# Kernel optimization log

Hardware: AMD Instinct MI355X
Metric: run time of the kernel (lower is better)

## Reference

```python
import jax, jax.numpy as jnp
import numpy as np

BN_EPS = 1e-3  # keras BatchNormalization default epsilon


def _conv(x, w):
    # x: [B,H,W,Cin], w: [kh,kw,Cin,Cout], stride 1, SAME padding
    return jax.lax.conv_general_dilated(
        x, w, window_strides=(1, 1), padding='SAME',
        dimension_numbers=('NHWC', 'HWIO', 'NHWC'))


def _bn(x, g, b, m, v):
    return (x - m) * jax.lax.rsqrt(v + BN_EPS) * g + b


def _pam(x, wq, bq, wk, bk, wv, bv, gamma):
    # Position attention: softmax over HW x HW similarity of 1x1-conv q/k.
    B, H, W, C = x.shape
    q = (_conv(x, wq) + bq).reshape(B, H * W, -1)   # [B,HW,C/8]
    k = (_conv(x, wk) + bk).reshape(B, H * W, -1)   # [B,HW,C/8]
    v = (_conv(x, wv) + bv).reshape(B, H * W, C)    # [B,HW,C]
    energy = jnp.einsum('bic,bjc->bij', q, k)       # [B,HW,HW]
    att = jax.nn.softmax(energy, axis=-1)
    out = jnp.einsum('bij,bjc->bic', att, v).reshape(B, H, W, C)
    return gamma * out + x


def _cam(x, gamma):
    # Channel attention with max-subtract stabilization, softmax over C.
    B, H, W, C = x.shape
    X = x.reshape(B, H * W, C)                      # channel-last flat
    energy = jnp.einsum('bnc,bnd->bcd', X, X)       # [B,C,C]
    energy_new = jnp.max(energy, axis=-1, keepdims=True) - energy
    att = jax.nn.softmax(energy_new, axis=-1)       # [B,C,C]
    out = jnp.einsum('bcd,bnd->bnc', att, X).reshape(B, H, W, C)
    return gamma * out + x


def setup_inputs() -> dict:
    key = jax.random.key(0)
    ks = jax.random.split(key, 16)
    B, H, W = 4, 64, 64
    Cin, Ci, Cq, Cout = 512, 128, 16, 19
    s = 0.05
    d = {
        'x': jax.random.normal(ks[0], (B, H, W, Cin), jnp.float32),
        'w5a': jax.random.normal(ks[1], (3, 3, Cin, Ci), jnp.float32) * s,
        'w5c': jax.random.normal(ks[2], (3, 3, Cin, Ci), jnp.float32) * s,
        'wq': jax.random.normal(ks[3], (1, 1, Ci, Cq), jnp.float32) * s,
        'bq': jnp.zeros((Cq,), jnp.float32),
        'wk': jax.random.normal(ks[4], (1, 1, Ci, Cq), jnp.float32) * s,
        'bk': jnp.zeros((Cq,), jnp.float32),
        'wv': jax.random.normal(ks[5], (1, 1, Ci, Ci), jnp.float32) * s,
        'bv': jnp.zeros((Ci,), jnp.float32),
        'pam_gamma': jnp.float32(0.5),
        'cam_gamma': jnp.float32(0.5),
        'w51': jax.random.normal(ks[6], (3, 3, Ci, Ci), jnp.float32) * s,
        'w52': jax.random.normal(ks[7], (3, 3, Ci, Ci), jnp.float32) * s,
        'w8': jax.random.normal(ks[8], (1, 1, Ci, Cout), jnp.float32) * s,
    }
    for i, nm in enumerate(['bn1', 'bn2', 'bn3', 'bn4']):
        d[nm + '_g'] = jnp.ones((Ci,), jnp.float32)
        d[nm + '_b'] = jnp.zeros((Ci,), jnp.float32)
        d[nm + '_m'] = jax.random.normal(ks[9 + i], (Ci,), jnp.float32) * 0.1
        d[nm + '_v'] = jnp.ones((Ci,), jnp.float32)
    return d


def reference(x, w5a, w5c, wq, bq, wk, bk, wv, bv, pam_gamma, cam_gamma,
              w51, w52, w8,
              bn1_g, bn1_b, bn1_m, bn1_v,
              bn2_g, bn2_b, bn2_m, bn2_v,
              bn3_g, bn3_b, bn3_m, bn3_v,
              bn4_g, bn4_b, bn4_m, bn4_v):
    # PAM branch
    feat1 = jax.nn.relu(_bn(_conv(x, w5a), bn1_g, bn1_b, bn1_m, bn1_v))
    sa_feat = _pam(feat1, wq, bq, wk, bk, wv, bv, pam_gamma)
    sa_conv = jax.nn.relu(_bn(_conv(sa_feat, w51), bn3_g, bn3_b, bn3_m, bn3_v))
    # CAM branch
    feat2 = jax.nn.relu(_bn(_conv(x, w5c), bn2_g, bn2_b, bn2_m, bn2_v))
    sc_feat = _cam(feat2, cam_gamma)
    sc_conv = jax.nn.relu(_bn(_conv(sc_feat, w52), bn4_g, bn4_b, bn4_m, bn4_v))
    # Fused output (dropout is identity at inference)
    feat_sum = sa_conv + sc_conv
    return _conv(feat_sum, w8)
```

## Files before the change

kernel.cpp:

```cpp
#include <hip/hip_runtime.h>
#include <hip/hip_bf16.h>
#include <math.h>

#define BN_EPS 1e-3f
#define LOG2E 1.44269504088896f

constexpr int Bn = 4, Hn = 64, Wn = 64, CIN = 512, CI = 128;
constexpr int HWn = Hn * Wn;
constexpr int NPIX = Bn * HWn;
constexpr int COn = 19;
constexpr int XSL = 66;
constexpr int XPG = XSL * 16;

struct F8 { float4 lo, hi; };

__device__ __forceinline__ F8 f8zero() {
    F8 r; r.lo = make_float4(0.f,0.f,0.f,0.f); r.hi = make_float4(0.f,0.f,0.f,0.f); return r;
}
__device__ __forceinline__ void fma8(F8 &acc, float a, const float4 &wlo, const float4 &whi) {
    acc.lo.x = fmaf(a, wlo.x, acc.lo.x);
    acc.lo.y = fmaf(a, wlo.y, acc.lo.y);
    acc.lo.z = fmaf(a, wlo.z, acc.lo.z);
    acc.lo.w = fmaf(a, wlo.w, acc.lo.w);
    acc.hi.x = fmaf(a, whi.x, acc.hi.x);
    acc.hi.y = fmaf(a, whi.y, acc.hi.y);
    acc.hi.z = fmaf(a, whi.z, acc.hi.z);
    acc.hi.w = fmaf(a, whi.w, acc.hi.w);
}

typedef __attribute__((ext_vector_type(8)))  short    short8;
typedef __attribute__((ext_vector_type(8)))  _Float16 half8;
typedef __attribute__((ext_vector_type(16))) float    f32x16;

__device__ __forceinline__ f32x16 f16z() {
    f32x16 z;
    #pragma unroll
    for (int i = 0; i < 16; ++i) z[i] = 0.f;
    return z;
}
__device__ __forceinline__ unsigned f2b(float f) {
    union { float f; unsigned u; } c; c.f = f;
    return (c.u + 0x7FFFu + ((c.u >> 16) & 1u)) >> 16;
}
__device__ __forceinline__ unsigned pack2(float lo, float hi) {
    return (f2b(hi) << 16) | f2b(lo);
}
__device__ __forceinline__ unsigned pkb2(float a, float b) {
    __hip_bfloat16 ha = __float2bfloat16(a);
    __hip_bfloat16 hb = __float2bfloat16(b);
    return ((unsigned)*(unsigned short*)&hb << 16) | *(unsigned short*)&ha;
}
__device__ __forceinline__ void split2(float a, float b, unsigned &hi, unsigned &lo) {
    const unsigned ha = f2b(a), hb = f2b(b);
    union { unsigned u; float f; } ua, ub; ua.u = ha << 16; ub.u = hb << 16;
    hi = (hb << 16) | ha;
    lo = pack2(a - ua.f, b - ub.f);
}
__device__ __forceinline__ unsigned pkh2(float a, float b) {
    union { _Float16 h; unsigned short u; } ca, cb;
    ca.h = (_Float16)a; cb.h = (_Float16)b;
    return ((unsigned)cb.u << 16) | ca.u;
}

__global__ __launch_bounds__(256)
void k_prep_w(const float* __restrict__ w5a, const float* __restrict__ w5c,
              const float* __restrict__ w51, const float* __restrict__ w52,
              char* __restrict__ wt1F, char* __restrict__ wt2aF, char* __restrict__ wt2bF)
{
    int idx = blockIdx.x * 256 + threadIdx.x;
    if (idx < 589824) {
        const int jp = idx & 7, co = (idx >> 3) & 255, ct = idx >> 11;
        const int tap = ct % 9, c = ct / 9;
        const float* src = (co < 128) ? w5a : w5c;
        const int coc = co & 127;
        const int ci = c*16 + jp*2;
        const float a = src[((size_t)tap*CIN + ci)*CI + coc];
        const float b = src[((size_t)tap*CIN + ci + 1)*CI + coc];
        const int L = co*32 + jp*4;
        *(unsigned*)(wt1F + (size_t)ct*8192 + L) = pkh2(a, b);
    } else {
        int k = idx - 589824;
        if (k >= 147456) return;
        const float* src = (k < 73728) ? w51 : w52;
        char* dstF = (k < 73728) ? wt2aF : wt2bF;
        if (k >= 73728) k -= 73728;
        const int jp = k & 7, co = (k >> 3) & 127, ct = k >> 10;
        const int tap = ct % 9, c = ct / 9;
        const int ci = c*16 + jp*2;
        const float a = src[((size_t)tap*CI + ci)*CI + co];
        const float b = src[((size_t)tap*CI + ci + 1)*CI + co];
        const int L = co*32 + jp*4;
        *(unsigned*)(dstF + (size_t)ct*4096 + L) = pkh2(a, b);
    }
}

__global__ __launch_bounds__(256)
void k_prep_bn(const float* g1, const float* b1, const float* m1, const float* v1,
               const float* g2, const float* b2, const float* m2, const float* v2,
               const float* g3, const float* b3, const float* m3, const float* v3,
               const float* g4, const float* b4, const float* m4, const float* v4,
               float* bnAs, float* bnAb, float* bnBs, float* bnBb)
{
    const int t = threadIdx.x, c = t & 127;
    {
        const float *g = (t < 128) ? g1 : g2, *b = (t < 128) ? b1 : b2;
        const float *m = (t < 128) ? m1 : m2, *v = (t < 128) ? v1 : v2;
        const float s = g[c] * rsqrtf(v[c] + BN_EPS);
        bnAs[t] = s; bnAb[t] = b[c] - m[c]*s;
    }
    {
        const float *g = (t < 128) ? g3 : g4, *b = (t < 128) ? b3 : b4;
        const float *m = (t < 128) ? m3 : m4, *v = (t < 128) ? v3 : v4;
        const float s = g[c] * rsqrtf(v[c] + BN_EPS);
        bnBs[t] = s; bnBb[t] = b[c] - m[c]*s;
    }
}

__global__ __launch_bounds__(256)
void k_prep_x(const float* __restrict__ x, _Float16* __restrict__ xcv)
{
    __shared__ float Xl[16*520];
    const int t = threadIdx.x;
    const int pb = blockIdx.x * 16;
    #pragma unroll
    for (int i = 0; i < 8; ++i) {
        const int u = t + i*256;
        const int px = u >> 7, c4 = (u & 127) * 4;
        *(float4*)&Xl[px*520 + c4] = *(const float4*)&x[(size_t)(pb + px)*CIN + c4];
    }
    __syncthreads();
    const int rowg = pb >> 6, pixb = pb & 63;
    #pragma unroll
    for (int i = 0; i < 8; ++i) {
        const int u = t + i*256;
        const int chunk = u >> 6, rem = u & 63;
        const int pl = rem >> 2, u4 = rem & 3;
        const float* src = &Xl[pl*520 + chunk*16 + u4*4];
        uint2 v;
        v.x = pkh2(src[0], src[1]);
        v.y = pkh2(src[2], src[3]);
        *(uint2*)&xcv[(((size_t)rowg*32 + chunk)*XSL + (pixb + pl + 1))*16 + u4*4] = v;
    }
    if (pixb == 0 && t < 64) {
        const int chunk = t >> 1, sl = (t & 1) * 65;
        uint4* dst = (uint4*)&xcv[(((size_t)rowg*32 + chunk)*XSL + sl)*16];
        uint4 z; z.x = 0u; z.y = 0u; z.z = 0u; z.w = 0u;
        dst[0] = z; dst[1] = z;
    }
}

__global__ __launch_bounds__(256)
void k_zhalo(_Float16* __restrict__ saf_h, _Float16* __restrict__ scf_h)
{
    const int idx = blockIdx.x * 256 + threadIdx.x;
    if (idx >= 8192) return;
    _Float16* arr = (idx & 4096) ? scf_h : saf_h;
    const int rem = idx & 4095;
    const int row = rem >> 4, chunk = (rem >> 1) & 7, sl = (rem & 1) * 65;
    uint4* dst = (uint4*)&arr[(((size_t)row*8 + chunk)*XSL + sl)*16];
    uint4 z; z.x = 0u; z.y = 0u; z.z = 0u; z.w = 0u;
    dst[0] = z; dst[1] = z;
}

template<int NCHNK, int NCOTOT, int WCOBASE>
__global__ __launch_bounds__(256)
void k_convl(const _Float16* __restrict__ xcv0, const _Float16* __restrict__ xcv1,
             const _Float16* __restrict__ wtF0, const _Float16* __restrict__ wtF1,
             const float* __restrict__ bnS, const float* __restrict__ bnBi,
             float* __restrict__ out0, float* __restrict__ out1)
{
    constexpr int WU4  = 1152;
    constexpr int XU4  = 396;
    constexpr int BUFB = (WU4 + XU4) * 16;
    __shared__ __align__(16) char Ls[2*BUFB];

    const int t    = threadIdx.x;
    const int wgid = blockIdx.x;
    const int xcd  = wgid & 7;
    const int sel  = xcd >> 2;
    const int ch2  = (xcd >> 1) & 1;
    const int row  = ((wgid >> 3) << 1) | (xcd & 1);
    const _Float16* xcv = sel ? xcv1 : xcv0;
    const _Float16* wtF = sel ? wtF1 : wtF0;
    float* dst = sel ? out1 : out0;

    const int hh = row & 63;
    const int dyLo = (hh == 0)  ? 1 : 0;
    const int dyHi = (hh == 63) ? 1 : 2;
    const int l = t & 63, w = t >> 6;
    const int lo5 = l & 31, hf = l >> 5;
    const int mi = w >> 1, nt = w & 1;
    const int cobase0 = WCOBASE*sel + ch2*64;

    bool sAct[7]; bool sIsW[7]; int sDst[7]; unsigned sSrc[7]; unsigned sStr[7];
    #pragma unroll
    for (int i = 0; i < 7; ++i) {
        const int u = t + i*256;
        sAct[i] = false; sIsW[i] = false; sDst[i] = -1; sSrc[i] = 0; sStr[i] = 0;
        if (u < WU4) {
            const int tap = u >> 7, rem = u & 127;
            sAct[i] = true; sIsW[i] = true;
            sSrc[i] = (unsigned)((tap*NCOTOT + cobase0)*32 + rem*16);
            sStr[i] = (unsigned)(9*NCOTOT*32);
            sDst[i] = (tap*128 + (rem & 1)*64 + (rem >> 1)) * 16;
        } else if (u < WU4 + XU4) {
            const int j = u - WU4;
            const int page = j / 132, rem132 = j - page*132;
            const int slot = rem132 >> 1, u4h = rem132 & 1;
            sAct[i] = (page >= dyLo && page <= dyHi);
            sSrc[i] = (unsigned)((((row + page - 1)*NCHNK)*XPG + slot*16 + u4h*8) * 2);
            sStr[i] = (unsigned)(XPG*2);
            sDst[i] = (WU4 + j) * 16;
        }
    }
    int xoff[3];
    #pragma unroll
    for (int dx = 0; dx < 3; ++dx)
        xoff[dx] = WU4*16 + ((mi*32 + lo5 + dx)*2 + hf)*16;
    const int wlane = (hf*64 + nt*32 + lo5)*16;

    f32x16 acc = f16z();

    uint4 xr[7];
    auto loadS = [&](int c) {
        #pragma unroll
        for (int i = 0; i < 7; ++i) {
            uint4 v; v.x = 0u; v.y = 0u; v.z = 0u; v.w = 0u;
            if (sAct[i]) {
                const char* base = sIsW[i] ? (const char*)wtF : (const char*)xcv;
                v = *(const uint4*)(base + (size_t)sSrc[i] + (size_t)c*sStr[i]);
            }
            xr[i] = v;
        }
    };

    loadS(0);
    int p = 0;
    for (int c = 0; c < NCHNK; ++c) {
        char* Lp = Ls + p*BUFB;
        #pragma unroll
        for (int i = 0; i < 7; ++i)
            if (sDst[i] >= 0) *(uint4*)(Lp + sDst[i]) = xr[i];
        __syncthreads();
        if (c + 1 < NCHNK) loadS(c + 1);
        #pragma unroll
        for (int dy = 0; dy < 3; ++dy) {
            if (dy < dyLo || dy > dyHi) continue;
            #pragma unroll
            for (int dx = 0; dx < 3; ++dx) {
                const half8 wf = *(const half8*)(Lp + ((dy*3 + dx)*128)*16 + wlane);
                const half8 xf = *(const half8*)(Lp + dy*(132*16) + xoff[dx]);
                acc = __builtin_amdgcn_mfma_f32_32x32x16_f16(wf, xf, acc, 0, 0, 0);
            }
        }
        p ^= 1;
    }
    const int px = mi*32 + lo5;
    const size_t pg = (size_t)row*Wn + px;
    #pragma unroll
    for (int r = 0; r < 16; ++r) {
        const int crow = (r & 3) + 8*(r >> 2) + 4*hf;
        const int och = ch2*64 + nt*32 + crow;
        const int bnidx = sel*128 + och;
        dst[pg*CI + och] = fmaxf(fmaf(acc[r], bnS[bnidx], bnBi[bnidx]), 0.f);
    }
}

__global__ __launch_bounds__(256)
void k_qk(const float* __restrict__ feat1,
          const float* __restrict__ wq, const float* __restrict__ bq,
          const float* __restrict__ wk, const float* __restrict__ bk,
          __hip_bfloat16* __restrict__ qb, __hip_bfloat16* __restrict__ kb)
{
    __shared__ float Al[64*129];
    __shared__ __align__(16) float Wl[128*32];
    const int t = threadIdx.x;
    const int pb = blockIdx.x * 64;
    for (int idx = t; idx < 64*128; idx += 256) {
        const int p = idx >> 7, ci = idx & 127;
        Al[p*129 + ci] = feat1[(size_t)(pb + p)*CI + ci];
    }
    for (int idx = t; idx < 128*32; idx += 256) {
        const int ci = idx >> 5, c = idx & 31;
        Wl[idx] = (c < 16) ? wq[ci*16 + c] : wk[ci*16 + (c - 16)];
    }
    __syncthreads();
    const int p = t & 63, cg = t >> 6, co = cg * 8;
    F8 acc = f8zero();
    #pragma unroll 8
    for (int ci = 0; ci < 128; ++ci) {
        const float a = Al[p*129 + ci];
        const float4 wlo = *(const float4*)&Wl[ci*32 + co];
        const float4 whi = *(const float4*)&Wl[ci*32 + co + 4];
        fma8(acc, a, wlo, whi);
    }
    const float* af = (const float*)&acc;
    #pragma unroll
    for (int j = 0; j < 8; ++j) {
        const int c = co + j;
        if (c < 16) qb[(size_t)(pb + p)*16 + c]        = __float2bfloat16((af[j] + bq[c]) * LOG2E);
        else        kb[(size_t)(pb + p)*16 + (c - 16)] = __float2bfloat16(af[j] + bk[c - 16]);
    }
}

__global__ __launch_bounds__(256)
void k_v(const float* __restrict__ feat1, const float* __restrict__ wv,
         const float* __restrict__ bv, __hip_bfloat16* __restrict__ vbT)
{
    __shared__ float Al[32*129];
    __shared__ __align__(16) float Wl[64*128];
    const int t = threadIdx.x;
    const int pb = blockIdx.x * 32;
    for (int idx = t; idx < 32*128; idx += 256) {
        const int p = idx >> 7, ci = idx & 127;
        Al[p*129 + ci] = feat1[(size_t)(pb + p)*CI + ci];
    }
    const int px = t & 15, co = (t >> 4) * 8;
    F8 acc0 = f8zero(), acc1 = f8zero();
    for (int ch = 0; ch < 2; ++ch) {
        __syncthreads();
        #pragma unroll
        for (int r = 0; r < 8; ++r) {
            const int i4 = t + r*256;
            const int kk = i4 >> 5, c4 = (i4 & 31) * 4;
            *(float4*)&Wl[kk*128 + c4] = *(const float4*)&wv[(size_t)(ch*64 + kk)*CI + c4];
        }
        __syncthreads();
        #pragma unroll 4
        for (int kk = 0; kk < 64; ++kk) {
            const float a0 = Al[px*129 + ch*64 + kk];
            const float a1 = Al[(px+16)*129 + ch*64 + kk];
            const float4 wlo = *(const float4*)&Wl[kk*128 + co];
            const float4 whi = *(const float4*)&Wl[kk*128 + co + 4];
            fma8(acc0, a0, wlo, whi);
            fma8(acc1, a1, wlo, whi);
        }
    }
    const int p0 = pb + px;
    const int bb = p0 / HWn, pin0 = p0 % HWn;
    const int k16a = pin0 >> 4, ko = pin0 & 15;
    const float* a0f = (const float*)&acc0;
    const float* a1f = (const float*)&acc1;
    #pragma unroll
    for (int j = 0; j < 8; ++j) {
        const int c = co + j;
        const size_t base = ((size_t)bb*256*CI*16) + (size_t)c*16 + ko;
        vbT[base + (size_t)k16a*CI*16]       = __float2bfloat16(a0f[j] + bv[c]);
        vbT[base + (size_t)(k16a + 1)*CI*16] = __float2bfloat16(a1f[j] + bv[c]);
    }
}

__global__ __launch_bounds__(256)
void k_pam(const __hip_bfloat16* __restrict__ qb, const __hip_bfloat16* __restrict__ kb,
           const __hip_bfloat16* __restrict__ vbT, const float* __restrict__ feat1,
           const float* __restrict__ gamma, _Float16* __restrict__ saf_h)
{
    __shared__ __align__(16) char pbuf[16896];
    __shared__ float msArr[4][32];
    __shared__ float ssArr[4][32];
    __shared__ float ssum[32];
    const int t  = threadIdx.x;
    const int wv = t >> 6, l = t & 63;
    const int lo5 = l & 31, h = l >> 5;
    unsigned* Ppk = (unsigned*)(pbuf + wv*4096);
    float* osum = (float*)pbuf;

    const int q0 = blockIdx.x * 32;
    const int bb = q0 / HWn;
    const size_t jb = (size_t)bb * HWn;
    const __hip_bfloat16* vbB = vbT + (size_t)bb * 256 * CI * 16;

    const short8 qfrag = *(const short8*)&qb[(size_t)(q0 + lo5)*16 + 8*h];
    const f32x16 zro = f16z();

    f32x16 o[4];
    #pragma unroll
    for (int cb = 0; cb < 4; ++cb) o[cb] = f16z();

    float m_run = -1e30f, s_run = 0.f;

    for (int k0 = wv*1024; k0 < wv*1024 + 1024; k0 += 64) {
        const short8 kf0 = *(const short8*)&kb[(jb + k0 +      lo5)*16 + 8*h];
        const short8 kf1 = *(const short8*)&kb[(jb + k0 + 32 + lo5)*16 + 8*h];
        short8 vf[4][4];
        #pragma unroll
        for (int s = 0; s < 4; ++s)
            #pragma unroll
            for (int cb = 0; cb < 4; ++cb)
                vf[s][cb] = *(const short8*)&vbB[
                    (((size_t)(k0 >> 4) + s)*CI + cb*32 + lo5)*16 + 8*h];

        f32x16 e0 = __builtin_amdgcn_mfma_f32_32x32x16_bf16(kf0, qfrag, zro, 0, 0, 0);
        f32x16 e1 = __builtin_amdgcn_mfma_f32_32x32x16_bf16(kf1, qfrag, zro, 0, 0, 0);

        float mt = fmaxf(e0[0], e1[0]);
        #pragma unroll
        for (int r = 1; r < 16; ++r) mt = fmaxf(mt, fmaxf(e0[r], e1[r]));
        mt = fmaxf(mt, __shfl_xor(mt, 32));

        if (__any(mt > m_run + 11.5416f)) {
            const float mnew = fmaxf(m_run, mt);
            const float sc = exp2f(m_run - mnew);
            s_run *= sc;
            #pragma unroll
            for (int cb = 0; cb < 4; ++cb)
                #pragma unroll
                for (int r = 0; r < 16; ++r) o[cb][r] *= sc;
            m_run = mnew;
        }

        #pragma unroll
        for (int r = 0; r < 16; ++r) {
            e0[r] = exp2f(e0[r] - m_run);
            e1[r] = exp2f(e1[r] - m_run);
        }
        float ss = 0.f;
        #pragma unroll
        for (int r = 0; r < 16; ++r) ss += e0[r] + e1[r];
        s_run += ss;

        #pragma unroll
        for (int r = 0; r < 16; r += 2) {
            const int pidx = ((r & 3) >> 1) + 4*(r >> 2) + 2*h;
            Ppk[pidx*32 + lo5]        = pkb2(e0[r], e0[r+1]);
            Ppk[(16 + pidx)*32 + lo5] = pkb2(e1[r], e1[r+1]);
        }
        #pragma unroll
        for (int s = 0; s < 4; ++s) {
            union { unsigned u[4]; short8 s8; } P;
            #pragma unroll
            for (int w = 0; w < 4; ++w)
                P.u[w] = Ppk[(s*8 + 4*h + w)*32 + lo5];
            #pragma unroll
            for (int cb = 0; cb < 4; ++cb)
                o[cb] = __builtin_amdgcn_mfma_f32_32x32x16_bf16(vf[s][cb], P.s8, o[cb], 0, 0, 0);
        }
    }

    const float s_w = s_run + __shfl_xor(s_run, 32);
    if (h == 0) { msArr[wv][lo5] = m_run; ssArr[wv][lo5] = s_w; }
    __syncthreads();

    float M = msArr[0][lo5];
    #pragma unroll
    for (int w = 1; w < 4; ++w) M = fmaxf(M, msArr[w][lo5]);
    float stot = 0.f;
    #pragma unroll
    for (int w = 0; w < 4; ++w) stot += exp2f(msArr[w][lo5] - M) * ssArr[w][lo5];
    if (wv == 0 && h == 0) ssum[lo5] = stot;
    const float myscale = exp2f(m_run - M);
    #pragma unroll
    for (int cb = 0; cb < 4; ++cb)
        #pragma unroll
        for (int r = 0; r < 16; ++r) o[cb][r] *= myscale;

    for (int w = 0; w < 4; ++w) {
        if (wv == w) {
            #pragma unroll
            for (int cb = 0; cb < 4; ++cb)
                #pragma unroll
                for (int r = 0; r < 16; ++r) {
                    const int c = cb*32 + (r & 3) + 8*(r >> 2) + 4*h;
                    float* p = &osum[lo5*132 + c];
                    if (w == 0) *p = o[cb][r]; else *p += o[cb][r];
                }
        }
        __syncthreads();
    }

    const float g = gamma[0];
    const int qloc = t >> 3, ch8 = t & 7;
    const float inv = 1.f / ssum[qloc];
    const int pgl = q0 + qloc;
    const int rowp = pgl >> 6, pixp = pgl & 63;
    const size_t gbase = (size_t)pgl*CI + ch8*16;
    union { _Float16 hv[16]; uint4 u[2]; } tmp;
    #pragma unroll
    for (int j = 0; j < 16; ++j)
        tmp.hv[j] = (_Float16)(g*(osum[qloc*132 + ch8*16 + j]*inv) + feat1[gbase + j]);
    uint4* dsth = (uint4*)&saf_h[(((size_t)rowp*8 + ch8)*XSL + (pixp + 1))*16];
    dsth[0] = tmp.u[0];
    dsth[1] = tmp.u[1];
}

__global__ __launch_bounds__(256)
void k_xpose(const float* __restrict__ feat2,
             char* __restrict__ f2TH, char* __restrict__ f2TL)
{
    __shared__ float Xl[64*129];
    const int t = threadIdx.x;
    const int pb = blockIdx.x * 64;
    const int bb = pb / HWn, pin = pb % HWn;
    for (int idx = t; idx < 64*128; idx += 256) {
        const int p = idx >> 7, ci = idx & 127;
        Xl[p*129 + ci] = feat2[(size_t)(pb + p)*CI + ci];
    }
    __syncthreads();
    const int c = t >> 1, half = t & 1;
    const size_t rowb = ((size_t)(bb*CI + c)*HWn + pin + half*32) * 2;
    #pragma unroll
    for (int j = 0; j < 16; ++j) {
        const float a = Xl[(half*32 + 2*j)*129 + c];
        const float b = Xl[(half*32 + 2*j + 1)*129 + c];
        unsigned hi, lo; split2(a, b, hi, lo);
        *(unsigned*)(f2TH + rowb + 4*j) = hi;
        *(unsigned*)(f2TL + rowb + 4*j) = lo;
    }
}

__global__ __launch_bounds__(256)
void k_cam_energy_m(const char* __restrict__ f2TH, const char* __restrict__ f2TL,
                    float* __restrict__ epart)
{
    __shared__ __align__(16) char Vh[128*256];
    __shared__ __align__(16) char Vl[128*256];
    const int t = threadIdx.x;
    const int ks = blockIdx.x, bb = blockIdx.y;
    const int l = t & 63, w = t >> 6;
    const int lo5 = l & 31, hf = l >> 5;

    #pragma unroll
    for (int pass = 0; pass < 8; ++pass) {
        const int slot = pass*256 + t;
        const int c = slot >> 4, g = slot & 15;
        const size_t gaddr = ((size_t)(bb*CI + c)*HWn + ks*128)*2 + g*16;
        const int laddr = c*256 + ((g*16) ^ ((c & 15) << 4));
        *(float4*)(Vh + laddr) = *(const float4*)(f2TH + gaddr);
        *(float4*)(Vl + laddr) = *(const float4*)(f2TL + gaddr);
    }
    __syncthreads();

    f32x16 acc[4];
    #pragma unroll
    for (int nj = 0; nj < 4; ++nj) acc[nj] = f16z();
    const int cA = w*32 + lo5;
    const int swA = (cA & 15) << 4;

    #pragma unroll
    for (int kk = 0; kk < 8; ++kk) {
        const int kb = kk*32 + hf*16;
        const short8 ah = *(const short8*)(Vh + cA*256 + (kb ^ swA));
        const short8 al = *(const short8*)(Vl + cA*256 + (kb ^ swA));
        #pragma unroll
        for (int nj = 0; nj < 4; ++nj) {
            const int dB = nj*32 + lo5;
            const int swB = (dB & 15) << 4;
            const short8 bh = *(const short8*)(Vh + dB*256 + (kb ^ swB));
            const short8 bl = *(const short8*)(Vl + dB*256 + (kb ^ swB));
            acc[nj] = __builtin_amdgcn_mfma_f32_32x32x16_bf16(ah, bh, acc[nj], 0, 0, 0);
            acc[nj] = __builtin_amdgcn_mfma_f32_32x32x16_bf16(al, bh, acc[nj], 0, 0, 0);
            acc[nj] = __builtin_amdgcn_mfma_f32_32x32x16_bf16(ah, bl, acc[nj], 0, 0, 0);
        }
    }
    float* ep = epart + ((size_t)(bb*32 + ks)*CI)*CI;
    #pragma unroll
    for (int nj = 0; nj < 4; ++nj)
        #pragma unroll
        for (int r = 0; r < 16; ++r) {
            const int c = w*32 + (r & 3) + 8*(r >> 2) + 4*hf;
            ep[(size_t)c*CI + nj*32 + lo5] = acc[nj][r];
        }
}

__global__ __launch_bounds__(64)
void k_cam_rs(const float* __restrict__ epart, float* __restrict__ att)
{
    const int lane = threadIdx.x;
    const int row = blockIdx.x;
    const int bb = row >> 7, c = row & 127;
    float2 e = make_float2(0.f, 0.f);
    for (int ks = 0; ks < 32; ++ks) {
        const float2 v = *(const float2*)&epart[
            ((size_t)(bb*32 + ks)*CI + c)*CI + lane*2];
        e.x += v.x; e.y += v.y;
    }
    float M = fmaxf(e.x, e.y);
    #pragma unroll
    for (int off = 32; off > 0; off >>= 1) M = fmaxf(M, __shfl_xor(M, off));
    const float en0 = M - e.x, en1 = M - e.y;
    float mx = fmaxf(en0, en1);
    #pragma unroll
    for (int off = 32; off > 0; off >>= 1) mx = fmaxf(mx, __shfl_xor(mx, off));
    const float p0 = __expf(en0 - mx), p1 = __expf(en1 - mx);
    float s = p0 + p1;
    #pragma unroll
    for (int off = 32; off > 0; off >>= 1) s += __shfl_xor(s, off);
    const float inv = 1.f / s;
    float2 o; o.x = p0*inv; o.y = p1*inv;
    *(float2*)&att[(size_t)row*CI + lane*2] = o;
}

__global__ __launch_bounds__(256)
void k_cam_apply(const float* __restrict__ feat2, const float* __restrict__ att,
                 const float* __restrict__ gamma, _Float16* __restrict__ scf_h)
{
    __shared__ float Xl[64*129];
    __shared__ __align__(16) float aT[128*64];
    const int t = threadIdx.x;
    const int pb = blockIdx.x * 64;
    const int bb = pb / HWn;
    const int ch = blockIdx.y * 64;
    for (int idx = t; idx < 64*128; idx += 256) {
        const int p = idx >> 7, ci = idx & 127;
        Xl[p*129 + ci] = feat2[(size_t)(pb + p)*CI + ci];
    }
    for (int idx = t; idx < 128*64; idx += 256) {
        const int d = idx >> 6, cc = idx & 63;
        aT[d*64 + cc] = att[((size_t)bb*CI + ch + cc)*CI + d];
    }
    __syncthreads();
    const int px = t & 63, cg = t >> 6;
    F8 accA = f8zero(), accB = f8zero();
    #pragma unroll 4
    for (int d = 0; d < 128; ++d) {
        const float xv = Xl[px*129 + d];
        const float* ap = &aT[d*64 + cg*16];
        const float4 a0 = *(const float4*)&ap[0];
        const float4 a1 = *(const float4*)&ap[4];
        const float4 a2 = *(const float4*)&ap[8];
        const float4 a3 = *(const float4*)&ap[12];
        fma8(accA, xv, a0, a1);
        fma8(accB, xv, a2, a3);
    }
    const float g = gamma[0];
    const float* fa = (const float*)&accA;
    const float* fb = (const float*)&accB;
    const int p0g = pb + px;
    const int rowA = p0g >> 6, pixA = p0g & 63;
    const int chunkA = (ch >> 4) + cg;
    const size_t baseA = (((size_t)rowA*8 + chunkA)*XSL + (pixA + 1))*16;
    #pragma unroll
    for (int j = 0; j < 8; ++j) {
        const int cA = ch + cg*16 + j;
        const int cB = cA + 8;
        scf_h[baseA + j]     = (_Float16)(g*fa[j] + Xl[px*129 + cA]);
        scf_h[baseA + 8 + j] = (_Float16)(g*fb[j] + Xl[px*129 + cB]);
    }
}

__global__ __launch_bounds__(256)
void k_final(const float* __restrict__ sa, const float* __restrict__ sc,
             const float* __restrict__ w8, float* __restrict__ out)
{
    __shared__ float Xl[64*129];
    __shared__ float w8l[128*COn];
    const int t = threadIdx.x;
    const int pb = blockIdx.x * 64;
    for (int idx = t; idx < 64*128; idx += 256) {
        const int p = idx >> 7, ci = idx & 127;
        const size_t gi = (size_t)(pb + p)*CI + ci;
        Xl[p*129 + ci] = sa[gi] + sc[gi];
    }
    for (int idx = t; idx < 128*COn; idx += 256) w8l[idx] = w8[idx];
    __syncthreads();
    for (int idx = t; idx < 64*COn; idx += 256) {
        const int p = idx / COn, co = idx - p*COn;
        float acc = 0.f;
        #pragma unroll 8
        for (int ci = 0; ci < 128; ++ci)
            acc = fmaf(Xl[p*129 + ci], w8l[ci*COn + co], acc);
        out[(size_t)(pb + p)*COn + co] = acc;
    }
}

extern "C" void kernel_launch(void* const* d_in, const int* in_sizes, int n_in,
                              void* d_out, int out_size, void* d_ws, size_t ws_size,
                              hipStream_t stream)
{
    const float* x    = (const float*)d_in[0];
    const float* w5a  = (const float*)d_in[1];
    const float* w5c  = (const float*)d_in[2];
    const float* wq   = (const float*)d_in[3];
    const float* bq   = (const float*)d_in[4];
    const float* wk   = (const float*)d_in[5];
    const float* bk   = (const float*)d_in[6];
    const float* wv   = (const float*)d_in[7];
    const float* bv   = (const float*)d_in[8];
    const float* pgam = (const float*)d_in[9];
    const float* cgam = (const float*)d_in[10];
    const float* w51  = (const float*)d_in[11];
    const float* w52  = (const float*)d_in[12];
    const float* w8   = (const float*)d_in[13];
    const float* bn1g = (const float*)d_in[14];
    const float* bn1b = (const float*)d_in[15];
    const float* bn1m = (const float*)d_in[16];
    const float* bn1v = (const float*)d_in[17];
    const float* bn2g = (const float*)d_in[18];
    const float* bn2b = (const float*)d_in[19];
    const float* bn2m = (const float*)d_in[20];
    const float* bn2v = (const float*)d_in[21];
    const float* bn3g = (const float*)d_in[22];
    const float* bn3b = (const float*)d_in[23];
    const float* bn3m = (const float*)d_in[24];
    const float* bn3v = (const float*)d_in[25];
    const float* bn4g = (const float*)d_in[26];
    const float* bn4b = (const float*)d_in[27];
    const float* bn4m = (const float*)d_in[28];
    const float* bn4v = (const float*)d_in[29];

    char* wsb = (char*)d_ws;
    float* feat1 = (float*)(wsb + 0);
    char*  f2TH  = wsb + 0;
    char*  f2TL  = wsb + 4194304;
    float* feat2 = (float*)(wsb + 8388608);
    _Float16* xcv   = (_Float16*)(wsb + 16777216);
    _Float16* saf_h = (_Float16*)(wsb + 16777216);
    _Float16* scf_h = (_Float16*)(wsb + 21102592);
    float*    epart = (float*)(wsb + 25427968);
    float* att = (float*)(wsb + 33816576);
    __hip_bfloat16* qb16 = (__hip_bfloat16*)(wsb + 34078720);
    __hip_bfloat16* kb16 = (__hip_bfloat16*)(wsb + 34603008);
    __hip_bfloat16* vbT  = (__hip_bfloat16*)(wsb + 35127296);
    char* wt1F  = wsb + 39321600;
    char* wt2aF = wsb + 41680896;
    char* wt2bF = wsb + 41975808;
    float* bnAs = (float*)(wsb + 42270720);
    float* bnAb = (float*)(wsb + 42271744);
    float* bnBs = (float*)(wsb + 42272768);
    float* bnBb = (float*)(wsb + 42273792);
    float* sa_conv = feat1;
    float* sc_conv = feat2;
    float* out  = (float*)d_out;

    k_prep_w<<<dim3(2880), 256, 0, stream>>>(w5a, w5c, w51, w52, wt1F, wt2aF, wt2bF);
    k_prep_bn<<<dim3(1), 256, 0, stream>>>(bn1g, bn1b, bn1m, bn1v, bn2g, bn2b, bn2m, bn2v,
                                           bn3g, bn3b, bn3m, bn3v, bn4g, bn4b, bn4m, bn4v,
                                           bnAs, bnAb, bnBs, bnBb);
    k_prep_x<<<dim3(1024), 256, 0, stream>>>(x, xcv);
    k_convl<32, 256, 128><<<dim3(1024), 256, 0, stream>>>(
        xcv, xcv, (const _Float16*)wt1F, (const _Float16*)wt1F, bnAs, bnAb, feat1, feat2);
    k_zhalo<<<dim3(32), 256, 0, stream>>>(saf_h, scf_h);
    k_qk<<<dim3(NPIX/64), 256, 0, stream>>>(feat1, wq, bq, wk, bk, qb16, kb16);
    k_v<<<dim3(NPIX/32), 256, 0, stream>>>(feat1, wv, bv, vbT);
    k_pam<<<dim3(NPIX/32), 256, 0, stream>>>(qb16, kb16, vbT, feat1, pgam, saf_h);
    k_xpose<<<dim3(NPIX/64), 256, 0, stream>>>(feat2, f2TH, f2TL);
    k_cam_energy_m<<<dim3(32, Bn), 256, 0, stream>>>(f2TH, f2TL, epart);
    k_cam_rs<<<dim3(Bn*CI), 64, 0, stream>>>(epart, att);
    k_cam_apply<<<dim3(NPIX/64, 2), 256, 0, stream>>>(feat2, att, cgam, scf_h);
    k_convl<8, 128, 0><<<dim3(1024), 256, 0, stream>>>(
        saf_h, scf_h, (const _Float16*)wt2aF, (const _Float16*)wt2bF,
        bnBs, bnBb, sa_conv, sc_conv);
    k_final<<<dim3(NPIX/64), 256, 0, stream>>>(sa_conv, sc_conv, w8, out);
}
```

Baseline: 244.2 us.

## Retile 3x3 conv kernel to four output rows per block with swizzled LDS

The implicit-GEMM 3x3 conv now runs 512-thread blocks, each computing four image rows for a 64-channel slice instead of one row, so each staged weight tile is reused across four rows and the input halo rows are shared. Each wave now produces two 32x32 MFMA accumulators, reusing one input fragment for two weight fragments. The LDS input layout gets an XOR swizzle to reduce bank conflicts. In exchange the grid shrinks to 256 blocks with more LDS and registers per block, which lowers the number of resident blocks and may leave CUs underused. Zero-padding rows are handled by skipping loads instead of skipping MFMAs.

```diff
diff --git a/kernel.cpp b/kernel.cpp
--- a/kernel.cpp
+++ b/kernel.cpp
@@ -163,72 +163,77 @@
 }
 
 template<int NCHNK, int NCOTOT, int WCOBASE>
-__global__ __launch_bounds__(256)
-void k_convl(const _Float16* __restrict__ xcv0, const _Float16* __restrict__ xcv1,
+__global__ __launch_bounds__(512)
+void k_convr(const _Float16* __restrict__ xcv0, const _Float16* __restrict__ xcv1,
              const _Float16* __restrict__ wtF0, const _Float16* __restrict__ wtF1,
              const float* __restrict__ bnS, const float* __restrict__ bnBi,
              float* __restrict__ out0, float* __restrict__ out1)
 {
     constexpr int WU4  = 1152;
-    constexpr int XU4  = 396;
+    constexpr int XU4  = 792;
     constexpr int BUFB = (WU4 + XU4) * 16;
     __shared__ __align__(16) char Ls[2*BUFB];
 
-    const int t    = threadIdx.x;
-    const int wgid = blockIdx.x;
-    const int xcd  = wgid & 7;
-    const int sel  = xcd >> 2;
-    const int ch2  = (xcd >> 1) & 1;
-    const int row  = ((wgid >> 3) << 1) | (xcd & 1);
+    const int t     = threadIdx.x;
+    const int wgid  = blockIdx.x;
+    const int slice = wgid & 3;
+    const int rg    = wgid >> 2;
+    const int sel   = slice >> 1;
+    const int ch2   = slice & 1;
     const _Float16* xcv = sel ? xcv1 : xcv0;
     const _Float16* wtF = sel ? wtF1 : wtF0;
     float* dst = sel ? out1 : out0;
 
-    const int hh = row & 63;
-    const int dyLo = (hh == 0)  ? 1 : 0;
-    const int dyHi = (hh == 63) ? 1 : 2;
+    const int hh0 = (rg*4) & 63;
     const int l = t & 63, w = t >> 6;
     const int lo5 = l & 31, hf = l >> 5;
-    const int mi = w >> 1, nt = w & 1;
+    const int r = w >> 1, mi = w & 1;
     const int cobase0 = WCOBASE*sel + ch2*64;
 
-    bool sAct[7]; bool sIsW[7]; int sDst[7]; unsigned sSrc[7]; unsigned sStr[7];
-    #pragma unroll
-    for (int i = 0; i < 7; ++i) {
-        const int u = t + i*256;
+    bool sAct[4]; bool sIsW[4]; int sDst[4]; size_t sSrc[4]; unsigned sStr[4];
+    #pragma unroll
+    for (int i = 0; i < 4; ++i) {
+        const int u = t + i*512;
         sAct[i] = false; sIsW[i] = false; sDst[i] = -1; sSrc[i] = 0; sStr[i] = 0;
         if (u < WU4) {
             const int tap = u >> 7, rem = u & 127;
+            const int co = rem >> 1, whf = rem & 1;
             sAct[i] = true; sIsW[i] = true;
-            sSrc[i] = (unsigned)((tap*NCOTOT + cobase0)*32 + rem*16);
+            sSrc[i] = (size_t)(tap*NCOTOT + cobase0 + co)*32 + whf*16;
             sStr[i] = (unsigned)(9*NCOTOT*32);
-            sDst[i] = (tap*128 + (rem & 1)*64 + (rem >> 1)) * 16;
+            sDst[i] = (tap*128 + whf*64 + co) * 16;
         } else if (u < WU4 + XU4) {
             const int j = u - WU4;
             const int page = j / 132, rem132 = j - page*132;
-            const int slot = rem132 >> 1, u4h = rem132 & 1;
-            sAct[i] = (page >= dyLo && page <= dyHi);
-            sSrc[i] = (unsigned)((((row + page - 1)*NCHNK)*XPG + slot*16 + u4h*8) * 2);
-            sStr[i] = (unsigned)(XPG*2);
-            sDst[i] = (WU4 + j) * 16;
-        }
-    }
-    int xoff[3];
-    #pragma unroll
-    for (int dx = 0; dx < 3; ++dx)
-        xoff[dx] = WU4*16 + ((mi*32 + lo5 + dx)*2 + hf)*16;
-    const int wlane = (hf*64 + nt*32 + lo5)*16;
-
-    f32x16 acc = f16z();
-
-    uint4 xr[7];
+            const int slot = rem132 >> 1, xhf = rem132 & 1;
+            const int hin = hh0 + page - 1;
+            sAct[i] = (hin >= 0 && hin < Hn);
+            const int gr = rg*4 + page - 1;
+            sSrc[i] = (size_t)gr*NCHNK*2112 + (size_t)(slot*32 + xhf*16);
+            sStr[i] = 2112u;
+            sDst[i] = WU4*16 + page*2112 + ((slot*32 + xhf*16) ^ ((slot & 7) << 4));
+        }
+    }
+    int xoff[3][3];
+    #pragma unroll
+    for (int dy = 0; dy < 3; ++dy)
+        #pragma unroll
+        for (int dx = 0; dx < 3; ++dx) {
+            const int s = mi*32 + lo5 + dx;
+            xoff[dy][dx] = WU4*16 + (r + dy)*2112 + ((s*32 + hf*16) ^ ((s & 7) << 4));
+        }
+
+    f32x16 acc[2];
+    acc[0] = f16z(); acc[1] = f16z();
+
+    uint4 xr[4];
     auto loadS = [&](int c) {
         #pragma unroll
-        for (int i = 0; i < 7; ++i) {
+        for (int i = 0; i < 4; ++i) {
             uint4 v; v.x = 0u; v.y = 0u; v.z = 0u; v.w = 0u;
             if (sAct[i]) {
                 const char* base = sIsW[i] ? (const char*)wtF : (const char*)xcv;
-                v = *(const uint4*)(base + (size_t)sSrc[i] + (size_t)c*sStr[i]);
+                v = *(const uint4*)(base + sSrc[i] + (size_t)c*sStr[i]);
             }
             xr[i] = v;
         }
@@ -239,31 +244,33 @@
     for (int c = 0; c < NCHNK; ++c) {
         char* Lp = Ls + p*BUFB;
         #pragma unroll
-        for (int i = 0; i < 7; ++i)
+        for (int i = 0; i < 4; ++i)
             if (sDst[i] >= 0) *(uint4*)(Lp + sDst[i]) = xr[i];
         __syncthreads();
         if (c + 1 < NCHNK) loadS(c + 1);
         #pragma unroll
-        for (int dy = 0; dy < 3; ++dy) {
-            if (dy < dyLo || dy > dyHi) continue;
+        for (int dy = 0; dy < 3; ++dy)
             #pragma unroll
             for (int dx = 0; dx < 3; ++dx) {
-                const half8 wf = *(const half8*)(Lp + ((dy*3 + dx)*128)*16 + wlane);
-                const half8 xf = *(const half8*)(Lp + dy*(132*16) + xoff[dx]);
-                acc = __builtin_amdgcn_mfma_f32_32x32x16_f16(wf, xf, acc, 0, 0, 0);
+                const half8 xf = *(const half8*)(Lp + xoff[dy][dx]);
+                const half8 w0 = *(const half8*)(Lp + ((dy*3 + dx)*128 + hf*64 + lo5)*16);
+                const half8 w1 = *(const half8*)(Lp + ((dy*3 + dx)*128 + hf*64 + 32 + lo5)*16);
+                acc[0] = __builtin_amdgcn_mfma_f32_32x32x16_f16(w0, xf, acc[0], 0, 0, 0);
+                acc[1] = __builtin_amdgcn_mfma_f32_32x32x16_f16(w1, xf, acc[1], 0, 0, 0);
             }
-        }
         p ^= 1;
     }
     const int px = mi*32 + lo5;
-    const size_t pg = (size_t)row*Wn + px;
-    #pragma unroll
-    for (int r = 0; r < 16; ++r) {
-        const int crow = (r & 3) + 8*(r >> 2) + 4*hf;
-        const int och = ch2*64 + nt*32 + crow;
-        const int bnidx = sel*128 + och;
-        dst[pg*CI + och] = fmaxf(fmaf(acc[r], bnS[bnidx], bnBi[bnidx]), 0.f);
-    }
+    const size_t pg = (size_t)(rg*4 + r)*Wn + px;
+    #pragma unroll
+    for (int cot = 0; cot < 2; ++cot)
+        #pragma unroll
+        for (int rr = 0; rr < 16; ++rr) {
+            const int crow = (rr & 3) + 8*(rr >> 2) + 4*hf;
+            const int och = ch2*64 + cot*32 + crow;
+            const int bnidx = sel*128 + och;
+            dst[pg*CI + och] = fmaxf(fmaf(acc[cot][rr], bnS[bnidx], bnBi[bnidx]), 0.f);
+        }
 }
 
 __global__ __launch_bounds__(256)
@@ -727,7 +734,7 @@
                                            bn3g, bn3b, bn3m, bn3v, bn4g, bn4b, bn4m, bn4v,
                                            bnAs, bnAb, bnBs, bnBb);
     k_prep_x<<<dim3(1024), 256, 0, stream>>>(x, xcv);
-    k_convl<32, 256, 128><<<dim3(1024), 256, 0, stream>>>(
+    k_convr<32, 256, 128><<<dim3(256), 512, 0, stream>>>(
         xcv, xcv, (const _Float16*)wt1F, (const _Float16*)wt1F, bnAs, bnAb, feat1, feat2);
     k_zhalo<<<dim3(32), 256, 0, stream>>>(saf_h, scf_h);
     k_qk<<<dim3(NPIX/64), 256, 0, stream>>>(feat1, wq, bq, wk, bk, qb16, kb16);
@@ -737,7 +744,7 @@
     k_cam_energy_m<<<dim3(32, Bn), 256, 0, stream>>>(f2TH, f2TL, epart);
     k_cam_rs<<<dim3(Bn*CI), 64, 0, stream>>>(epart, att);
     k_cam_apply<<<dim3(NPIX/64, 2), 256, 0, stream>>>(feat2, att, cgam, scf_h);
-    k_convl<8, 128, 0><<<dim3(1024), 256, 0, stream>>>(
+    k_convr<8, 128, 0><<<dim3(256), 512, 0, stream>>>(
         saf_h, scf_h, (const _Float16*)wt2aF, (const _Float16*)wt2bF,
         bnBs, bnBb, sa_conv, sc_conv);
     k_final<<<dim3(NPIX/64), 256, 0, stream>>>(sa_conv, sc_conv, w8, out);
```

Result: faster. 216.7 us (-11.2%).
